# Optimization experiments

Measured on AMD Instinct MI355X. Metric: run time of the kernel, lower is better.

The kernel has to match this reference:

```python
import jax, jax.numpy as jnp
import numpy as np
import math

B, S, E, H = 4096, 10, 1536, 12
HD = E // H
SCALE = HD ** -0.5
LN_EPS = 1e-5


def make_pe(d_model=E, max_len=S):
    pos = np.arange(max_len, dtype=np.float32)[:, None]
    div = np.exp(np.arange(0, d_model, 2, dtype=np.float32) * (-math.log(10000.0) / d_model))
    pe = np.zeros((max_len, d_model), dtype=np.float32)
    pe[:, 0::2] = np.sin(pos * div)
    pe[:, 1::2] = np.cos(pos * div)
    return jnp.asarray(pe)


def setup_inputs() -> dict:
    key = jax.random.key(0)
    ks = jax.random.split(key, 10)
    inp = {
        "a_vectors": jax.random.normal(ks[0], (B, S, E), jnp.float32),
        "b_vectors": jax.random.normal(ks[1], (B, S, E), jnp.float32),
    }
    # prefix-valid masks: True = padding (as the torch module expects)
    len_a = jax.random.randint(ks[2], (B,), 1, S + 1)
    len_b = jax.random.randint(ks[3], (B,), 1, S + 1)
    pos = jnp.arange(S)
    inp["mask_a"] = pos[None, :] >= len_a[:, None]
    inp["mask_b"] = pos[None, :] >= len_b[:, None]
    # learned params: weights stored [in, out]; y = x @ W + b
    for i, name in enumerate(["q", "k", "v", "o", "f"]):
        kw = jax.random.fold_in(ks[4], i)
        inp[name + "_w"] = jax.random.normal(kw, (E, E), jnp.float32) * (E ** -0.5)
        inp[name + "_b"] = jnp.zeros((E,), jnp.float32)
    inp["ln_g"] = jnp.ones((E,), jnp.float32)
    inp["ln_b"] = jnp.zeros((E,), jnp.float32)
    return inp


def _layernorm(x, g, b):
    mu = jnp.mean(x, axis=-1, keepdims=True)
    var = jnp.mean((x - mu) ** 2, axis=-1, keepdims=True)
    return (x - mu) * jax.lax.rsqrt(var + LN_EPS) * g + b


def _branch(x, mask, q_w, q_b, k_w, k_b, v_w, v_b, o_w, o_b, f_w, f_b, ln_g, ln_b, pe):
    # dropout is identity (eval mode)
    x = _layernorm(x + pe[None, :, :], ln_g, ln_b)          # [B,S,E]
    # gather last valid vector (prefix-valid mask)
    last_idx = jnp.sum(~mask, axis=1) - 1                    # [B]
    last = jnp.take_along_axis(x, last_idx[:, None, None], axis=1)[:, 0, :]  # [B,E]
    q = (last @ q_w + q_b).reshape(B, H, HD)                 # [B,H,HD]
    k = (x @ k_w + k_b).reshape(B, S, H, HD)                 # [B,S,H,HD]
    v = (x @ v_w + v_b).reshape(B, S, H, HD)
    scores = jnp.einsum("bhd,bshd->bhs", q, k) * SCALE       # [B,H,S]
    scores = jnp.where(mask[:, None, :], -1e9, scores)
    w = jax.nn.softmax(scores, axis=-1)
    ctx = jnp.einsum("bhs,bshd->bhd", w, v).reshape(B, E)    # [B,E]
    out = ctx @ o_w + o_b
    return jax.nn.gelu(out @ f_w + f_b, approximate=False)   # [B,E]


def reference(a_vectors, b_vectors, mask_a, mask_b,
              q_w, q_b, k_w, k_b, v_w, v_b, o_w, o_b, f_w, f_b, ln_g, ln_b):
    pe = make_pe()
    params = (q_w, q_b, k_w, k_b, v_w, v_b, o_w, o_b, f_w, f_b, ln_g, ln_b, pe)
    a_rep = _branch(a_vectors, mask_a, *params)
    b_rep = _branch(b_vectors, mask_b, *params)
    return (a_rep, b_rep)
```

## Files before the change

### kernel.cpp

```cpp
#include <hip/hip_runtime.h>
#include <math.h>

#define BB 4096
#define SS 10
#define EE 1536
#define HH 12
#define HDIM 128
#define MROWS (BB * SS)
#define BB2 (2 * BB)
#define MROWS2 (2 * MROWS)

typedef short short8 __attribute__((ext_vector_type(8)));
typedef float f32x4 __attribute__((ext_vector_type(4)));
typedef const unsigned char __attribute__((address_space(1))) gu8;
typedef unsigned char __attribute__((address_space(3))) lu8;

__device__ __forceinline__ unsigned short f2bf(float x) {
  unsigned int u = __float_as_uint(x);
  return (unsigned short)((u + 0x7FFFu + ((u >> 16) & 1u)) >> 16);
}
__device__ __forceinline__ float bf2f(unsigned short u) {
  return __uint_as_float(((unsigned int)u) << 16);
}

__global__ void k_detect(const unsigned char* __restrict__ m, int* __restrict__ flag) {
  __shared__ int fb, ff;
  if (threadIdx.x == 0) { fb = 0; ff = 0; }
  __syncthreads();
  int lb = 0, lf = 0;
  for (int j = threadIdx.x; j < BB * SS; j += blockDim.x) {
    unsigned char v = m[j];
    if (v) {
      int r = j & 3;
      if (r == 1) lb = 1;
      else if (r >= 2) lf = 1;
    }
  }
  if (lb) atomicOr(&fb, 1);
  if (lf) atomicOr(&ff, 1);
  __syncthreads();
  if (threadIdx.x == 0) *flag = fb ? 1 : (ff ? 2 : 0);
}

__global__ void k_lastidx(const void* __restrict__ ma, const void* __restrict__ mb,
                          const int* __restrict__ flag, int* __restrict__ lastidx) {
  int idx = blockIdx.x * blockDim.x + threadIdx.x;
  if (idx >= BB2) return;
  const void* m = (idx >= BB) ? mb : ma;
  int b = idx & (BB - 1);
  int f = *flag;
  int len = 0;
  for (int s = 0; s < SS; ++s) {
    int j = b * SS + s;
    int pad;
    if (f == 1)      pad = ((const unsigned char*)m)[j] != 0;
    else if (f == 2) pad = ((const float*)m)[j] != 0.0f;
    else             pad = ((const int*)m)[j] != 0;
    len += (pad == 0);
  }
  lastidx[idx] = len - 1;
}

__global__ void k_pe(float* __restrict__ pe) {
  int idx = blockIdx.x * blockDim.x + threadIdx.x;
  if (idx >= SS * EE) return;
  int s = idx / EE, e = idx - (idx / EE) * EE;
  float fe = (float)(e & ~1);
  float freq = expf(fe * (-9.210340371976184f / (float)EE));
  float arg = (float)s * freq;
  pe[idx] = (e & 1) ? cosf(arg) : sinf(arg);
}

__global__ void k_trans(const float* __restrict__ w0, const float* __restrict__ w1,
                        const float* __restrict__ w2, const float* __restrict__ w3,
                        const float* __restrict__ w4, unsigned short* __restrict__ wt) {
  __shared__ float tile[32][33];
  int z = blockIdx.z;
  const float* W = z == 0 ? w0 : z == 1 ? w1 : z == 2 ? w2 : z == 3 ? w3 : w4;
  unsigned short* T = wt + (size_t)z * EE * EE;
  int n0 = blockIdx.x * 32, k0 = blockIdx.y * 32;
  int tx = threadIdx.x, ty = threadIdx.y;
#pragma unroll
  for (int i = 0; i < 4; ++i)
    tile[ty + i * 8][tx] = W[(size_t)(k0 + ty + i * 8) * EE + n0 + tx];
  __syncthreads();
#pragma unroll
  for (int i = 0; i < 4; ++i)
    T[(size_t)(n0 + ty + i * 8) * EE + k0 + tx] = f2bf(tile[tx][ty + i * 8]);
}

__global__ void k_cast(const float* __restrict__ in, unsigned short* __restrict__ out) {
  int i = (blockIdx.x * blockDim.x + threadIdx.x) * 8;
  if (i >= EE * EE) return;
  float4 a = *(const float4*)(in + i);
  float4 b = *(const float4*)(in + i + 4);
  short8 v;
  v[0] = (short)f2bf(a.x); v[1] = (short)f2bf(a.y);
  v[2] = (short)f2bf(a.z); v[3] = (short)f2bf(a.w);
  v[4] = (short)f2bf(b.x); v[5] = (short)f2bf(b.y);
  v[6] = (short)f2bf(b.z); v[7] = (short)f2bf(b.w);
  *(short8*)(out + i) = v;
}

__global__ __launch_bounds__(256) void k_ln(
    const float* __restrict__ av, const float* __restrict__ bv,
    const float* __restrict__ pe,
    const float* __restrict__ g, const float* __restrict__ be,
    const int* __restrict__ lastidx,
    unsigned short* __restrict__ xln, unsigned short* __restrict__ lastx) {
  int w = threadIdx.x >> 6, lane = threadIdx.x & 63;
  int row = blockIdx.x * 4 + w;
  const float* xin = (row < MROWS) ? (av + (size_t)row * EE)
                                   : (bv + (size_t)(row - MROWS) * EE);
  int bg = row / SS, s = row - bg * SS;
  const float4* x4 = (const float4*)xin;
  const float4* p4 = (const float4*)(pe + s * EE);
  float4 v[6];
  float s1 = 0.f, s2 = 0.f;
#pragma unroll
  for (int j = 0; j < 6; ++j) {
    float4 a = x4[j * 64 + lane], p = p4[j * 64 + lane];
    a.x += p.x; a.y += p.y; a.z += p.z; a.w += p.w;
    v[j] = a;
    s1 += a.x + a.y + a.z + a.w;
    s2 += a.x * a.x + a.y * a.y + a.z * a.z + a.w * a.w;
  }
#pragma unroll
  for (int off = 32; off; off >>= 1) {
    s1 += __shfl_xor(s1, off, 64);
    s2 += __shfl_xor(s2, off, 64);
  }
  float mu = s1 * (1.0f / EE);
  float var = s2 * (1.0f / EE) - mu * mu;
  float scl = rsqrtf(var + 1e-5f);
  bool isLast = (s == lastidx[bg]);
  uint2* orow = (uint2*)(xln + (size_t)row * EE);
  uint2* lrow = (uint2*)(lastx + (size_t)bg * EE);
  const float4* g4 = (const float4*)g;
  const float4* b4 = (const float4*)be;
#pragma unroll
  for (int j = 0; j < 6; ++j) {
    int idx = j * 64 + lane;
    float4 gg = g4[idx], bb = b4[idx];
    float o0 = (v[j].x - mu) * scl * gg.x + bb.x;
    float o1 = (v[j].y - mu) * scl * gg.y + bb.y;
    float o2 = (v[j].z - mu) * scl * gg.z + bb.z;
    float o3 = (v[j].w - mu) * scl * gg.w + bb.w;
    uint2 pk;
    pk.x = (unsigned int)f2bf(o0) | ((unsigned int)f2bf(o1) << 16);
    pk.y = (unsigned int)f2bf(o2) | ((unsigned int)f2bf(o3) << 16);
    orow[idx] = pk;
    if (isLast) lrow[idx] = pk;
  }
}

__global__ __launch_bounds__(256) void k_gemm_g(
    const unsigned short* __restrict__ A, int aStrH, int lda,
    const unsigned short* __restrict__ Bt, int bStrH, int ldb,
    const float* __restrict__ bias, int biasStrH,
    void* __restrict__ C, int cStrH, int ldc,
    int MB, int NB, int K) {
  __shared__ __align__(16) unsigned char smA[8192];
  __shared__ __align__(16) unsigned char smB[8192];
  int h = blockIdx.y;
  const unsigned char* Ab = (const unsigned char*)(A + (size_t)h * aStrH);
  const unsigned char* Bb = (const unsigned char*)(Bt + (size_t)h * bStrH);
  const float* bi = bias ? bias + (size_t)h * biasStrH : nullptr;
  int per = MB >> 3;
  int bid = blockIdx.x;
  int xcd = bid & 7, lin = bid >> 3;
  int mt = xcd * per + lin / NB;
  int nt = lin % NB;
  int m0 = mt << 7, n0 = nt << 7;
  int tid = threadIdx.x, wid = tid >> 6, lane = tid & 63;
  int wm = wid >> 1, wn = wid & 1;
  f32x4 acc[4][4] = {};
  const size_t ldaB = (size_t)lda * 2, ldbB = (size_t)ldb * 2;
  int lrow = lane & 15, kgrp = lane >> 4;
  int aoff = (wm * 64 + lrow) * 64 + kgrp * 16;
  int boff = (wn * 64 + lrow) * 64 + kgrp * 16;
  int Lbase = wid * 1024 + lane * 16;
  const int nk = K >> 5;
  for (int kt = 0; kt < nk; ++kt) {
    int k0b = kt << 6;
#pragma unroll
    for (int issue = 0; issue < 2; ++issue) {
      int L = issue * 4096 + Lbase;
      int row = L >> 6, colb = L & 63;
      int Lu = issue * 4096 + wid * 1024;
      __builtin_amdgcn_global_load_lds((gu8*)(Ab + (size_t)(m0 + row) * ldaB + k0b + colb),
                                       (lu8*)(smA + Lu), 16, 0, 0);
      __builtin_amdgcn_global_load_lds((gu8*)(Bb + (size_t)(n0 + row) * ldbB + k0b + colb),
                                       (lu8*)(smB + Lu), 16, 0, 0);
    }
    __syncthreads();
    short8 af[4], bfr[4];
#pragma unroll
    for (int i = 0; i < 4; ++i) {
      af[i]  = *(const short8*)(smA + aoff + i * 1024);
      bfr[i] = *(const short8*)(smB + boff + i * 1024);
    }
#pragma unroll
    for (int mi = 0; mi < 4; ++mi)
#pragma unroll
      for (int ni = 0; ni < 4; ++ni)
        acc[mi][ni] = __builtin_amdgcn_mfma_f32_16x16x32_bf16(af[mi], bfr[ni], acc[mi][ni], 0, 0, 0);
    __syncthreads();
  }
  int rbase = m0 + wm * 64 + (lane >> 4) * 4;
  int cbase = n0 + wn * 64 + (lane & 15);
#pragma unroll
  for (int mi = 0; mi < 4; ++mi) {
#pragma unroll
    for (int ni = 0; ni < 4; ++ni) {
      int c = cbase + ni * 16;
      float bv = bi ? bi[c] : 0.f;
#pragma unroll
      for (int j = 0; j < 4; ++j) {
        int r = rbase + mi * 16 + j;
        float val = acc[mi][ni][j] + bv;
        ((unsigned short*)C)[(size_t)h * cStrH + (size_t)r * ldc + c] = f2bf(val);
      }
    }
  }
}

#define MMAQ(AR_, BR_, QM, QN)                                                  \
  do {                                                                          \
    _Pragma("unroll")                                                           \
    for (int mi_ = 0; mi_ < 4; ++mi_) {                                         \
      _Pragma("unroll")                                                         \
      for (int ni_ = 0; ni_ < 2; ++ni_) {                                       \
        acc[(QM)*4 + mi_][(QN)*2 + ni_] = __builtin_amdgcn_mfma_f32_16x16x32_bf16( \
            AR_[mi_][0], BR_[ni_][0], acc[(QM)*4 + mi_][(QN)*2 + ni_], 0, 0, 0);   \
        acc[(QM)*4 + mi_][(QN)*2 + ni_] = __builtin_amdgcn_mfma_f32_16x16x32_bf16( \
            AR_[mi_][1], BR_[ni_][1], acc[(QM)*4 + mi_][(QN)*2 + ni_], 0, 0, 0);   \
      }                                                                         \
    }                                                                           \
  } while (0)

#define PHASE_MID()                                      \
  do {                                                   \
    __builtin_amdgcn_s_barrier();                        \
    asm volatile("s_waitcnt lgkmcnt(0)" ::: "memory");   \
    __builtin_amdgcn_s_setprio(1);                       \
  } while (0)
#define PHASE_END()                                      \
  do {                                                   \
    __builtin_amdgcn_s_setprio(0);                       \
    __builtin_amdgcn_s_barrier();                        \
  } while (0)

template<int EPI>
__global__ __launch_bounds__(512, 2) void k_gemm256(
    const unsigned short* __restrict__ A, const unsigned short* __restrict__ Bt,
    const float* __restrict__ bias,
    void* __restrict__ C, int M, int N, int K) {
  __shared__ __align__(16) unsigned char lds[131072];
  const int NT = K >> 6;
  const int niters = NT >> 1;
  const int Ntiles = N >> 8;
  const int perx = (M >> 8) >> 3;
  const int MTG = 4;
  int bid = blockIdx.x;
  int xcd = bid & 7, lin = bid >> 3;
  int grp = lin / (MTG * Ntiles);
  int rem = lin - grp * (MTG * Ntiles);
  int nt = rem / MTG, mi_ = rem - nt * MTG;
  int mt = xcd * perx + grp * MTG + mi_;
  int m0 = mt << 8, n0 = nt << 8;
  int tid = threadIdx.x;
  int w = tid >> 6, lane = tid & 63;
  int wm = w >> 2, wn = w & 3;
  const size_t lda = (size_t)K * 2;
  const unsigned char* Ag = (const unsigned char*)A;
  const unsigned char* Bg = (const unsigned char*)Bt;

  unsigned char* A0 = lds;
  unsigned char* B0 = lds + 32768;
  unsigned char* A1 = lds + 65536;
  unsigned char* B1 = lds + 98304;

  int lrows = lane >> 3;
  int colswz = (((lane & 7) ^ (lrows & 7)) << 4);
  int rowA = w * 8;
  int rowB = (w >> 2) * 64 + (w & 3) * 8;

  auto stageA = [&](unsigned char* ldsA, int q, int kt) {
    int cb = kt * 128 + colswz;
#pragma unroll
    for (int i = 0; i < 2; ++i) {
      int tr = q * 64 + i * 128 + rowA;
      __builtin_amdgcn_global_load_lds(
          (gu8*)(Ag + (size_t)(m0 + tr + lrows) * lda + cb),
          (lu8*)(ldsA + tr * 128), 16, 0, 0);
    }
  };
  auto stageB = [&](unsigned char* ldsB, int q, int kt) {
    int cb = kt * 128 + colswz;
#pragma unroll
    for (int i = 0; i < 2; ++i) {
      int tr = q * 32 + i * 128 + rowB;
      __builtin_amdgcn_global_load_lds(
          (gu8*)(Bg + (size_t)(n0 + tr + lrows) * lda + cb),
          (lu8*)(ldsB + tr * 128), 16, 0, 0);
    }
  };

  int lrow = lane & 15, kgrp = lane >> 4, r7 = lane & 7;
  int s0 = ((kgrp ^ r7) << 4), s1 = (((kgrp | 4) ^ r7) << 4);
  int abase = (wm * 128 + lrow) * 128;
  int bbase = (wn * 64 + lrow) * 128;

  short8 ar[4][2], br0[2][2], br1[2][2];
  f32x4 acc[8][4];
#pragma unroll
  for (int i = 0; i < 8; ++i)
#pragma unroll
    for (int j = 0; j < 4; ++j) acc[i][j] = (f32x4)0.f;

  auto ldA = [&](unsigned char* ldsA, int qm) {
#pragma unroll
    for (int mi2 = 0; mi2 < 4; ++mi2) {
      ar[mi2][0] = *(const short8*)(ldsA + abase + qm * 8192 + mi2 * 2048 + s0);
      ar[mi2][1] = *(const short8*)(ldsA + abase + qm * 8192 + mi2 * 2048 + s1);
    }
  };
  auto ldB = [&](unsigned char* ldsB, int qn, short8 (&br)[2][2]) {
#pragma unroll
    for (int ni2 = 0; ni2 < 2; ++ni2) {
      br[ni2][0] = *(const short8*)(ldsB + bbase + qn * 4096 + ni2 * 2048 + s0);
      br[ni2][1] = *(const short8*)(ldsB + bbase + qn * 4096 + ni2 * 2048 + s1);
    }
  };

  stageA(A0, 0, 0); stageB(B0, 0, 0); stageA(A0, 1, 0); stageB(B0, 1, 0);
  stageA(A1, 0, 1); stageB(B1, 0, 1);
  asm volatile("s_waitcnt vmcnt(8)" ::: "memory");
  __builtin_amdgcn_s_barrier();

  for (int it = 0; it < niters - 1; ++it) {
    int t1 = 2 * it + 1, t2 = 2 * it + 2, t3 = 2 * it + 3;
    ldA(A0, 0); ldB(B0, 0, br0);
    stageA(A1, 1, t1);
    asm volatile("s_waitcnt vmcnt(6)" ::: "memory");
    PHASE_MID(); MMAQ(ar, br0, 0, 0); PHASE_END();
    ldB(B0, 1, br1);
    stageB(B1, 1, t1);
    PHASE_MID(); MMAQ(ar, br1, 0, 1); PHASE_END();
    ldA(A0, 1);
    stageA(A0, 0, t2);
    PHASE_MID(); MMAQ(ar, br0, 1, 0); PHASE_END();
    stageB(B0, 0, t2);
    asm volatile("s_waitcnt vmcnt(8)" ::: "memory");
    PHASE_MID(); MMAQ(ar, br1, 1, 1); PHASE_END();
    ldA(A1, 0); ldB(B1, 0, br0);
    stageA(A0, 1, t2);
    asm volatile("s_waitcnt vmcnt(6)" ::: "memory");
    PHASE_MID(); MMAQ(ar, br0, 0, 0); PHASE_END();
    ldB(B1, 1, br1);
    stageB(B0, 1, t2);
    PHASE_MID(); MMAQ(ar, br1, 0, 1); PHASE_END();
    ldA(A1, 1);
    if (t3 < NT) stageA(A1, 0, t3);
    PHASE_MID(); MMAQ(ar, br0, 1, 0); PHASE_END();
    if (t3 < NT) stageB(B1, 0, t3);
    asm volatile("s_waitcnt vmcnt(8)" ::: "memory");
    PHASE_MID(); MMAQ(ar, br1, 1, 1); PHASE_END();
  }
  {
    int t1 = NT - 1;
    ldA(A0, 0); ldB(B0, 0, br0);
    stageA(A1, 1, t1);
    asm volatile("s_waitcnt vmcnt(6)" ::: "memory");
    PHASE_MID(); MMAQ(ar, br0, 0, 0); PHASE_END();
    ldB(B0, 1, br1);
    stageB(B1, 1, t1);
    PHASE_MID(); MMAQ(ar, br1, 0, 1); PHASE_END();
    ldA(A0, 1);
    PHASE_MID(); MMAQ(ar, br0, 1, 0); PHASE_END();
    asm volatile("s_waitcnt vmcnt(4)" ::: "memory");
    PHASE_MID(); MMAQ(ar, br1, 1, 1); PHASE_END();
    ldA(A1, 0); ldB(B1, 0, br0);
    asm volatile("s_waitcnt vmcnt(2)" ::: "memory");
    PHASE_MID(); MMAQ(ar, br0, 0, 0); PHASE_END();
    ldB(B1, 1, br1);
    asm volatile("s_waitcnt vmcnt(0)" ::: "memory");
    PHASE_MID(); MMAQ(ar, br1, 0, 1); PHASE_END();
    ldA(A1, 1);
    PHASE_MID(); MMAQ(ar, br0, 1, 0); PHASE_END();
    PHASE_MID(); MMAQ(ar, br1, 1, 1); PHASE_END();
  }

  int rb = m0 + wm * 128 + (lane >> 4) * 4;
  int cb2 = n0 + wn * 64 + (lane & 15);
#pragma unroll
  for (int fm = 0; fm < 8; ++fm)
#pragma unroll
    for (int fn = 0; fn < 4; ++fn) {
      int c = cb2 + fn * 16;
      float bv = bias[c];
#pragma unroll
      for (int j = 0; j < 4; ++j) {
        int r = rb + fm * 16 + j;
        float val = acc[fm][fn][j] + bv;
        if (EPI == 2) {
          val = 0.5f * val * (1.0f + erff(val * 0.7071067811865476f));
          ((float*)C)[(size_t)r * N + c] = val;
        } else {
          ((unsigned short*)C)[(size_t)r * N + c] = f2bf(val);
        }
      }
    }
}

__global__ __launch_bounds__(256) void k_attn2(
    const unsigned short* __restrict__ xln,
    unsigned short* qky,
    const int* __restrict__ lastidx) {
  __shared__ __align__(16) unsigned short xs[10 * 1544];
  __shared__ float swp[4 * 256];
  __shared__ float scf[120];
  __shared__ float wsm[120];
  int b = blockIdx.x;
  int t = threadIdx.x;
  const unsigned short* xg = xln + (size_t)b * SS * EE;
  unsigned short* qg = qky + (size_t)b * HH * EE;
#pragma unroll
  for (int j = 0; j < 8; ++j) {
    int idx = t + j * 256;
    if (idx < 1920) {
      int row = idx / 192, col = (idx - row * 192) * 8;
      *(short8*)(xs + row * 1544 + col) = *(const short8*)(xg + row * 1536 + col);
    }
  }
  __syncthreads();
  int w = t >> 6, lane = t & 63;
  {
    int hr = lane & 15; if (hr > 11) hr = 11;
    int sr = lane & 15; if (sr > 9) sr = 9;
    int kg = lane >> 4;
    f32x4 pacc = (f32x4)0.f;
#pragma unroll
    for (int kt = 0; kt < 12; ++kt) {
      int k0 = w * 384 + kt * 32 + kg * 8;
      short8 a  = *(const short8*)(qg + hr * 1536 + k0);
      short8 bf = *(const short8*)(xs + sr * 1544 + k0);
      pacc = __builtin_amdgcn_mfma_f32_16x16x32_bf16(a, bf, pacc, 0, 0, 0);
    }
    int prow = (lane >> 4) * 4, pcol = lane & 15;
#pragma unroll
    for (int j = 0; j < 4; ++j)
      swp[w * 256 + (prow + j) * 16 + pcol] = pacc[j];
  }
  __syncthreads();
  if (t < 120) {
    int h = t / 10, s = t - (t / 10) * 10;
    float v = swp[h * 16 + s] + swp[256 + h * 16 + s] +
              swp[512 + h * 16 + s] + swp[768 + h * 16 + s];
    scf[t] = v * 0.08838834764831845f;
  }
  __syncthreads();
  int li = lastidx[b];
  if (t < 12) {
    float mx = -1e30f;
    for (int s = 0; s <= li; ++s) mx = fmaxf(mx, scf[t * 10 + s]);
    float sum = 0.f;
    for (int s = 0; s <= li; ++s) {
      float e = expf(scf[t * 10 + s] - mx);
      wsm[t * 10 + s] = e; sum += e;
    }
    float inv = 1.0f / sum;
    for (int s = 0; s <= li; ++s) wsm[t * 10 + s] *= inv;
  }
  __syncthreads();
  float wv[3][10];
#pragma unroll
  for (int hl = 0; hl < 3; ++hl)
#pragma unroll
    for (int s = 0; s < 10; ++s)
      wv[hl][s] = (s <= li) ? wsm[(3 * w + hl) * 10 + s] : 0.f;
#pragma unroll
  for (int pass = 0; pass < 12; ++pass) {
    int e0 = pass * 128 + lane * 2;
    float acc[3][2] = {};
    for (int s = 0; s <= li; ++s) {
      unsigned int x2 = *(const unsigned int*)(xs + s * 1544 + e0);
      float xlo = bf2f((unsigned short)(x2 & 0xffff));
      float xhi = bf2f((unsigned short)(x2 >> 16));
#pragma unroll
      for (int hl = 0; hl < 3; ++hl) {
        acc[hl][0] += wv[hl][s] * xlo;
        acc[hl][1] += wv[hl][s] * xhi;
      }
    }
#pragma unroll
    for (int hl = 0; hl < 3; ++hl) {
      unsigned int pk = (unsigned int)f2bf(acc[hl][0]) | ((unsigned int)f2bf(acc[hl][1]) << 16);
      *(unsigned int*)(qg + (3 * w + hl) * 1536 + e0) = pk;
    }
  }
}

extern "C" void kernel_launch(void* const* d_in, const int* in_sizes, int n_in,
                              void* d_out, int out_size, void* d_ws, size_t ws_size,
                              hipStream_t stream) {
  (void)in_sizes; (void)n_in; (void)out_size; (void)ws_size;
  const float* av  = (const float*)d_in[0];
  const float* bv  = (const float*)d_in[1];
  const void*  ma  = d_in[2];
  const void*  mb  = d_in[3];
  const float* qw  = (const float*)d_in[4];
  const float* qb  = (const float*)d_in[5];
  const float* kw  = (const float*)d_in[6];
  const float* kb  = (const float*)d_in[7];  (void)kb;
  const float* vw  = (const float*)d_in[8];
  const float* vbs = (const float*)d_in[9];
  const float* ow  = (const float*)d_in[10];
  const float* ob  = (const float*)d_in[11];
  const float* fw  = (const float*)d_in[12];
  const float* fbs = (const float*)d_in[13];
  const float* lng = (const float*)d_in[14];
  const float* lnb = (const float*)d_in[15];

  unsigned char* ws = (unsigned char*)d_ws;
  size_t off = 0;
  auto alloc = [&](size_t bytes) {
    size_t r = off; off = (off + bytes + 255) & ~(size_t)255; return (void*)(ws + r);
  };
  int* flag             = (int*)alloc(4);
  float* pe             = (float*)alloc((size_t)SS * EE * 4);
  unsigned short* wt    = (unsigned short*)alloc((size_t)5 * EE * EE * 2);
  unsigned short* kwb   = (unsigned short*)alloc((size_t)EE * EE * 2);
  int* lastidx          = (int*)alloc((size_t)BB2 * 4);
  unsigned short* xln   = (unsigned short*)alloc((size_t)MROWS2 * EE * 2);
  unsigned short* lastx = (unsigned short*)alloc((size_t)BB2 * EE * 2);
  unsigned short* qbuf  = (unsigned short*)alloc((size_t)BB2 * EE * 2);
  unsigned short* qky   = (unsigned short*)alloc((size_t)BB2 * HH * EE * 2);
  unsigned short* ctx   = (unsigned short*)alloc((size_t)BB2 * EE * 2);
  unsigned short* o1    = (unsigned short*)alloc((size_t)BB2 * EE * 2);

  unsigned short* wt_q = wt;
  unsigned short* wt_v = wt + (size_t)2 * EE * EE;
  unsigned short* wt_o = wt + (size_t)3 * EE * EE;
  unsigned short* wt_f = wt + (size_t)4 * EE * EE;

  k_detect<<<1, 256, 0, stream>>>((const unsigned char*)ma, flag);
  k_pe<<<(SS * EE + 255) / 256, 256, 0, stream>>>(pe);
  k_trans<<<dim3(EE / 32, EE / 32, 5), dim3(32, 8), 0, stream>>>(qw, kw, vw, ow, fw, wt);
  k_cast<<<(EE * EE / 8 + 255) / 256, 256, 0, stream>>>(kw, kwb);
  k_lastidx<<<(BB2 + 255) / 256, 256, 0, stream>>>(ma, mb, flag, lastidx);

  k_ln<<<MROWS2 / 4, 256, 0, stream>>>(av, bv, pe, lng, lnb, lastidx, xln, lastx);
  k_gemm256<0><<<(BB2 / 256) * (EE / 256), 512, 0, stream>>>(
      lastx, wt_q, qb, qbuf, BB2, EE, EE);
  k_gemm_g<<<dim3(64 * 12, HH), 256, 0, stream>>>(
      qbuf, HDIM, EE, kwb, HDIM, EE, nullptr, 0, qky, EE, HH * EE, 64, 12, HDIM);
  k_attn2<<<BB2, 256, 0, stream>>>(xln, qky, lastidx);
  k_gemm_g<<<dim3(64 * 1, HH), 256, 0, stream>>>(
      qky, EE, HH * EE, wt_v, (size_t)0 + HDIM * EE, EE, vbs, HDIM,
      ctx, HDIM, EE, 64, 1, EE);
  k_gemm256<0><<<(BB2 / 256) * (EE / 256), 512, 0, stream>>>(
      ctx, wt_o, ob, o1, BB2, EE, EE);
  k_gemm256<2><<<(BB2 / 256) * (EE / 256), 512, 0, stream>>>(
      o1, wt_f, fbs, d_out, BB2, EE, EE);
}
```

Baseline: 906.0 us.

## Read attention inputs from global memory instead of LDS and parallelize mask detection

The attention kernel no longer stages the 10x1536 bf16 token rows into shared memory. It reads them straight from global memory (through cache) for both the score MFMA and the weighted sum, and adds a min-blocks occupancy hint now that LDS use is much smaller. Score and softmax buffers are merged, and the weighted sum now loads all 10 rows unconditionally, relying on zero weights for padded positions. Mask-type detection now runs across 40 blocks with word-wide loads and global atomics after a memset, replacing one serial block. The risks are more global/L2 traffic and redundant loads of padded rows.

```diff
diff --git a/kernel.cpp b/kernel.cpp
--- a/kernel.cpp
+++ b/kernel.cpp
@@ -23,32 +23,25 @@
   return __uint_as_float(((unsigned int)u) << 16);
 }
 
-__global__ void k_detect(const unsigned char* __restrict__ m, int* __restrict__ flag) {
-  __shared__ int fb, ff;
-  if (threadIdx.x == 0) { fb = 0; ff = 0; }
-  __syncthreads();
+__global__ void k_detect(const unsigned int* __restrict__ m, int* __restrict__ flags) {
   int lb = 0, lf = 0;
-  for (int j = threadIdx.x; j < BB * SS; j += blockDim.x) {
-    unsigned char v = m[j];
-    if (v) {
-      int r = j & 3;
-      if (r == 1) lb = 1;
-      else if (r >= 2) lf = 1;
-    }
-  }
-  if (lb) atomicOr(&fb, 1);
-  if (lf) atomicOr(&ff, 1);
-  __syncthreads();
-  if (threadIdx.x == 0) *flag = fb ? 1 : (ff ? 2 : 0);
+  int stride = gridDim.x * blockDim.x;
+  for (int i = blockIdx.x * blockDim.x + threadIdx.x; i < BB * SS / 4; i += stride) {
+    unsigned int wv = m[i];
+    if ((wv >> 8) & 0xFFu) lb = 1;
+    if (wv >> 16) lf = 1;
+  }
+  if (lb) atomicOr(&flags[0], 1);
+  if (lf) atomicOr(&flags[1], 1);
 }
 
 __global__ void k_lastidx(const void* __restrict__ ma, const void* __restrict__ mb,
-                          const int* __restrict__ flag, int* __restrict__ lastidx) {
+                          const int* __restrict__ flags, int* __restrict__ lastidx) {
   int idx = blockIdx.x * blockDim.x + threadIdx.x;
   if (idx >= BB2) return;
   const void* m = (idx >= BB) ? mb : ma;
   int b = idx & (BB - 1);
-  int f = *flag;
+  int f = flags[0] ? 1 : (flags[1] ? 2 : 0);
   int len = 0;
   for (int s = 0; s < SS; ++s) {
     int j = b * SS + s;
@@ -414,38 +407,28 @@
     }
 }
 
-__global__ __launch_bounds__(256) void k_attn2(
+__global__ __launch_bounds__(256, 5) void k_attn2(
     const unsigned short* __restrict__ xln,
     unsigned short* qky,
     const int* __restrict__ lastidx) {
-  __shared__ __align__(16) unsigned short xs[10 * 1544];
   __shared__ float swp[4 * 256];
-  __shared__ float scf[120];
   __shared__ float wsm[120];
   int b = blockIdx.x;
   int t = threadIdx.x;
   const unsigned short* xg = xln + (size_t)b * SS * EE;
   unsigned short* qg = qky + (size_t)b * HH * EE;
-#pragma unroll
-  for (int j = 0; j < 8; ++j) {
-    int idx = t + j * 256;
-    if (idx < 1920) {
-      int row = idx / 192, col = (idx - row * 192) * 8;
-      *(short8*)(xs + row * 1544 + col) = *(const short8*)(xg + row * 1536 + col);
-    }
-  }
-  __syncthreads();
   int w = t >> 6, lane = t & 63;
+  int li = lastidx[b];
   {
     int hr = lane & 15; if (hr > 11) hr = 11;
     int sr = lane & 15; if (sr > 9) sr = 9;
     int kg = lane >> 4;
     f32x4 pacc = (f32x4)0.f;
-#pragma unroll
+#pragma unroll 4
     for (int kt = 0; kt < 12; ++kt) {
       int k0 = w * 384 + kt * 32 + kg * 8;
       short8 a  = *(const short8*)(qg + hr * 1536 + k0);
-      short8 bf = *(const short8*)(xs + sr * 1544 + k0);
+      short8 bf = *(const short8*)(xg + sr * 1536 + k0);
       pacc = __builtin_amdgcn_mfma_f32_16x16x32_bf16(a, bf, pacc, 0, 0, 0);
     }
     int prow = (lane >> 4) * 4, pcol = lane & 15;
@@ -458,20 +441,20 @@
     int h = t / 10, s = t - (t / 10) * 10;
     float v = swp[h * 16 + s] + swp[256 + h * 16 + s] +
               swp[512 + h * 16 + s] + swp[768 + h * 16 + s];
-    scf[t] = v * 0.08838834764831845f;
+    wsm[t] = v * 0.08838834764831845f;
   }
   __syncthreads();
-  int li = lastidx[b];
   if (t < 12) {
     float mx = -1e30f;
-    for (int s = 0; s <= li; ++s) mx = fmaxf(mx, scf[t * 10 + s]);
+    for (int s = 0; s <= li; ++s) mx = fmaxf(mx, wsm[t * 10 + s]);
     float sum = 0.f;
+    float ex[SS];
     for (int s = 0; s <= li; ++s) {
-      float e = expf(scf[t * 10 + s] - mx);
-      wsm[t * 10 + s] = e; sum += e;
+      ex[s] = expf(wsm[t * 10 + s] - mx);
+      sum += ex[s];
     }
     float inv = 1.0f / sum;
-    for (int s = 0; s <= li; ++s) wsm[t * 10 + s] *= inv;
+    for (int s = 0; s <= li; ++s) wsm[t * 10 + s] = ex[s] * inv;
   }
   __syncthreads();
   float wv[3][10];
@@ -480,14 +463,18 @@
 #pragma unroll
     for (int s = 0; s < 10; ++s)
       wv[hl][s] = (s <= li) ? wsm[(3 * w + hl) * 10 + s] : 0.f;
-#pragma unroll
+#pragma unroll 2
   for (int pass = 0; pass < 12; ++pass) {
     int e0 = pass * 128 + lane * 2;
+    unsigned int xr[10];
+#pragma unroll
+    for (int s = 0; s < 10; ++s)
+      xr[s] = *(const unsigned int*)(xg + s * 1536 + e0);
     float acc[3][2] = {};
-    for (int s = 0; s <= li; ++s) {
-      unsigned int x2 = *(const unsigned int*)(xs + s * 1544 + e0);
-      float xlo = bf2f((unsigned short)(x2 & 0xffff));
-      float xhi = bf2f((unsigned short)(x2 >> 16));
+#pragma unroll
+    for (int s = 0; s < 10; ++s) {
+      float xlo = bf2f((unsigned short)(xr[s] & 0xffff));
+      float xhi = bf2f((unsigned short)(xr[s] >> 16));
 #pragma unroll
       for (int hl = 0; hl < 3; ++hl) {
         acc[hl][0] += wv[hl][s] * xlo;
@@ -528,7 +515,7 @@
   auto alloc = [&](size_t bytes) {
     size_t r = off; off = (off + bytes + 255) & ~(size_t)255; return (void*)(ws + r);
   };
-  int* flag             = (int*)alloc(4);
+  int* flags            = (int*)alloc(8);
   float* pe             = (float*)alloc((size_t)SS * EE * 4);
   unsigned short* wt    = (unsigned short*)alloc((size_t)5 * EE * EE * 2);
   unsigned short* kwb   = (unsigned short*)alloc((size_t)EE * EE * 2);
@@ -545,11 +532,12 @@
   unsigned short* wt_o = wt + (size_t)3 * EE * EE;
   unsigned short* wt_f = wt + (size_t)4 * EE * EE;
 
-  k_detect<<<1, 256, 0, stream>>>((const unsigned char*)ma, flag);
+  hipMemsetAsync(flags, 0, 8, stream);
+  k_detect<<<40, 256, 0, stream>>>((const unsigned int*)ma, flags);
   k_pe<<<(SS * EE + 255) / 256, 256, 0, stream>>>(pe);
   k_trans<<<dim3(EE / 32, EE / 32, 5), dim3(32, 8), 0, stream>>>(qw, kw, vw, ow, fw, wt);
   k_cast<<<(EE * EE / 8 + 255) / 256, 256, 0, stream>>>(kw, kwb);
-  k_lastidx<<<(BB2 + 255) / 256, 256, 0, stream>>>(ma, mb, flag, lastidx);
+  k_lastidx<<<(BB2 + 255) / 256, 256, 0, stream>>>(ma, mb, flags, lastidx);
 
   k_ln<<<MROWS2 / 4, 256, 0, stream>>>(av, bv, pe, lng, lnb, lastidx, xln, lastx);
   k_gemm256<0><<<(BB2 / 256) * (EE / 256), 512, 0, stream>>>(
```

After: 1.045 ms. 15.3% more time.
